# Optimization experiments

Measured on AMD Instinct MI355X. Metric: run time of the kernel, lower is better.

Reference implementation:

```python
import jax, jax.numpy as jnp
import numpy as np
import math

D = 2048
NH = 16
HD = D // NH
MULT = 4
EPS = 1e-6


def rmsnorm(x, g):
    norm = jax.lax.rsqrt(jnp.mean(x * x, axis=-1, keepdims=True) + EPS)
    return g * x * norm


def setup_inputs() -> dict:
    key = jax.random.key(0)
    ks = jax.random.split(key, 8)
    s = 0.02  # keep activations in a sane range
    return {
        "x": jax.random.normal(ks[0], (2, 2048, D), dtype=jnp.float32),
        "g1": jnp.ones((D,), dtype=jnp.float32),
        "wq": jax.random.normal(ks[1], (D, D), dtype=jnp.float32) * s,
        "wk": jax.random.normal(ks[2], (D, D), dtype=jnp.float32) * s,
        "wv": jax.random.normal(ks[3], (D, D), dtype=jnp.float32) * s,
        "wo": jax.random.normal(ks[4], (D, D), dtype=jnp.float32) * s,
        "g2": jnp.ones((D,), dtype=jnp.float32),
        "w_up": jax.random.normal(ks[5], (2 * D * MULT, D), dtype=jnp.float32) * s,
        "w_down": jax.random.normal(ks[6], (D, D * MULT), dtype=jnp.float32) * s,
    }


def reference(x, g1, wq, wk, wv, wo, g2, w_up, w_down):
    B, T, _ = x.shape
    # --- causal self-attention with pre-RMSNorm ---
    h = rmsnorm(x, g1)
    q = (h @ wq.T).reshape(B, T, NH, HD).transpose(0, 2, 1, 3)  # [B,H,T,hd]
    k = (h @ wk.T).reshape(B, T, NH, HD).transpose(0, 2, 1, 3)
    v = (h @ wv.T).reshape(B, T, NH, HD).transpose(0, 2, 1, 3)
    att = jnp.einsum("bhtd,bhsd->bhts", q, k) / math.sqrt(HD)  # [B,H,T,T]
    neg = jnp.finfo(att.dtype).min
    causal = jnp.triu(jnp.full((T, T), neg, dtype=att.dtype), k=1)
    att = att + causal
    w = jax.nn.softmax(att, axis=-1)
    z = jnp.einsum("bhts,bhsd->bhtd", w, v)  # [B,H,T,hd]
    z = z.transpose(0, 2, 1, 3).reshape(B, T, D)
    x = x + z @ wo.T
    # --- SwiGLU-style FFN (GELU gate) with pre-RMSNorm ---
    h2 = rmsnorm(x, g2)
    uv = h2 @ w_up.T  # [B,T,2*D*MULT]
    u, vgate = jnp.split(uv, 2, axis=-1)
    ff = (jax.nn.gelu(u, approximate=False) * vgate) @ w_down.T
    return x + ff
```

## Files before the change

kernel.cpp:

```cpp
#include <hip/hip_runtime.h>
#include <math.h>

typedef __bf16 bf16_t;
typedef __bf16 bf16x8 __attribute__((ext_vector_type(8)));
typedef __bf16 bf16x4 __attribute__((ext_vector_type(4)));
typedef float f32x4 __attribute__((ext_vector_type(4)));

#define D_MODEL 2048
#define N_HEADS 16
#define HEAD_D 128
#define SEQ 2048
#define NTOK 4096
#define DFF 8192
#define UPN 16384

#define GLDS16(g, l) __builtin_amdgcn_global_load_lds( \
    (const __attribute__((address_space(1))) void*)(g), \
    (__attribute__((address_space(3))) void*)(l), 16, 0, 0)

#define MFMA16(a, b, c) __builtin_amdgcn_mfma_f32_16x16x32_bf16((a), (b), (c), 0, 0, 0)

__global__ __launch_bounds__(256) void cvt_bf16_kernel(const float* __restrict__ in,
                                                       bf16_t* __restrict__ out, long n4) {
    long i = (long)blockIdx.x * 256 + threadIdx.x;
    long stride = (long)gridDim.x * 256;
    for (; i < n4; i += stride) {
        float4 f = ((const float4*)in)[i];
        bf16x4 v;
        v[0] = (bf16_t)f.x; v[1] = (bf16_t)f.y; v[2] = (bf16_t)f.z; v[3] = (bf16_t)f.w;
        ((bf16x4*)out)[i] = v;
    }
}

__global__ __launch_bounds__(256) void rmsnorm_kernel(const float* __restrict__ x,
                                                      const float* __restrict__ g,
                                                      bf16_t* __restrict__ out) {
    int row = blockIdx.x;
    const float* xr = x + (size_t)row * D_MODEL;
    int c0 = threadIdx.x * 8;
    float4 a = *(const float4*)&xr[c0];
    float4 b = *(const float4*)&xr[c0 + 4];
    float ss = a.x*a.x + a.y*a.y + a.z*a.z + a.w*a.w
             + b.x*b.x + b.y*b.y + b.z*b.z + b.w*b.w;
    #pragma unroll
    for (int off = 1; off < 64; off <<= 1) ss += __shfl_xor(ss, off);
    __shared__ float red[4];
    if ((threadIdx.x & 63) == 0) red[threadIdx.x >> 6] = ss;
    __syncthreads();
    float norm = rsqrtf((red[0] + red[1] + red[2] + red[3]) * (1.f / D_MODEL) + 1e-6f);
    float4 ga = *(const float4*)&g[c0];
    float4 gb = *(const float4*)&g[c0 + 4];
    bf16x8 o;
    o[0] = (bf16_t)(a.x * ga.x * norm); o[1] = (bf16_t)(a.y * ga.y * norm);
    o[2] = (bf16_t)(a.z * ga.z * norm); o[3] = (bf16_t)(a.w * ga.w * norm);
    o[4] = (bf16_t)(b.x * gb.x * norm); o[5] = (bf16_t)(b.y * gb.y * norm);
    o[6] = (bf16_t)(b.z * gb.z * norm); o[7] = (bf16_t)(b.w * gb.w * norm);
    *(bf16x8*)&out[(size_t)row * D_MODEL + c0] = o;
}

__global__ __launch_bounds__(256) void combine3_kernel(const float* __restrict__ r,
        const float* __restrict__ p0, const float* __restrict__ p1,
        float* __restrict__ out, long n4) {
    long i = (long)blockIdx.x * 256 + threadIdx.x;
    long stride = (long)gridDim.x * 256;
    for (; i < n4; i += stride) {
        float4 a = ((const float4*)r)[i];
        float4 b = ((const float4*)p0)[i];
        float4 c = ((const float4*)p1)[i];
        float4 o; o.x = a.x+b.x+c.x; o.y = a.y+b.y+c.y; o.z = a.z+b.z+c.z; o.w = a.w+b.w+c.w;
        ((float4*)out)[i] = o;
    }
}

template<int MODE, int KSPLIT>
__global__ __launch_bounds__(512, 2)
void gemm256(const bf16_t* __restrict__ A, const bf16_t* __restrict__ W,
             void* __restrict__ o0, void* __restrict__ o1, void* __restrict__ o2,
             const float* __restrict__ res, int nbx, int K)
{
    __shared__ __align__(16) bf16_t ldsA[4 * 8192];
    __shared__ __align__(16) bf16_t ldsB[4 * 8192];
    const int tid = threadIdx.x;
    const int wave = tid >> 6, lane = tid & 63;
    const int lr = lane & 15, lg = lane >> 4;
    const int wm = wave >> 2, wn = wave & 3;

    const int nwg = gridDim.x, bid = blockIdx.x;
    const int cpx = nwg >> 3;
    const int s = (bid & 7) * cpx + (bid >> 3);
    const int by = s & 15, bx = s >> 4;
    const int bm0 = by * 256;
    const int bn0 = (MODE == 2) ? bx * 128 : bx * 256;
    const int z = (KSPLIT == 2) ? blockIdx.z : 0;
    const int Keff = K / KSPLIT;
    const int koff = z * Keff;

    const int rl0 = wave * 16 + (lane >> 2);
    const int Lof = ((lane & 3) ^ ((rl0 >> 1) & 3)) * 8;
    const bf16_t* asrc0 = A + (size_t)(bm0 + rl0) * K + koff + Lof;
    const bf16_t* asrc1 = asrc0 + (size_t)128 * K;
    const bf16_t* bsrc0;
    const bf16_t* bsrc1;
    if constexpr (MODE == 2) {
        int grp = rl0 >> 6, wi = rl0 & 63;
        int brow = (wi < 32) ? (bn0 + grp * 32 + wi) : (DFF + bn0 + grp * 32 + (wi - 32));
        bsrc0 = W + (size_t)brow * K + koff + Lof;
        bsrc1 = bsrc0 + (size_t)64 * K;
    } else {
        bsrc0 = W + (size_t)(bn0 + rl0) * K + koff + Lof;
        bsrc1 = bsrc0 + (size_t)128 * K;
    }

    auto issueA = [&](int t, int kh) {
        char* dst = (char*)ldsA + (((t & 1) * 2 + kh) * 16384) + wave * 1024;
        const bf16_t* sp = asrc0 + (size_t)t * 64 + kh * 32;
        GLDS16(sp, dst);
        GLDS16(asrc1 + (size_t)t * 64 + kh * 32, dst + 8192);
    };
    auto issueB = [&](int t, int kh) {
        char* dst = (char*)ldsB + (((t & 1) * 2 + kh) * 16384) + wave * 1024;
        GLDS16(bsrc0 + (size_t)t * 64 + kh * 32, dst);
        GLDS16(bsrc1 + (size_t)t * 64 + kh * 32, dst + 8192);
    };

    f32x4 acc[8][4] = {};
    const int xg = (lg ^ ((lr >> 1) & 3)) * 8;
    const int arow = wm * 128 + lr;
    const int brow = wn * 64 + lr;
    const int NKT = Keff >> 6;

    issueA(0, 0); issueB(0, 0); issueA(0, 1); issueB(0, 1);

#define HALF_BODY(J, ISSUE, KH, WC)                                                     \
    {                                                                                   \
        bf16x8 af[8], bfr[2];                                                           \
        const bf16_t* Ar = ldsA + (((J) & 1) * 2 + (KH)) * 8192;                        \
        const bf16_t* Br = ldsB + (((J) & 1) * 2 + (KH)) * 8192;                        \
        if (ISSUE) issueA((J) + 1, (KH));                                               \
        asm volatile("s_waitcnt vmcnt(" WC ")" ::: "memory");                           \
        __builtin_amdgcn_s_barrier();                                                   \
        _Pragma("unroll")                                                               \
        for (int m = 0; m < 8; ++m) af[m] = *(const bf16x8*)&Ar[(arow + m * 16) * 32 + xg]; \
        _Pragma("unroll")                                                               \
        for (int n = 0; n < 2; ++n) bfr[n] = *(const bf16x8*)&Br[(brow + n * 16) * 32 + xg]; \
        __builtin_amdgcn_s_setprio(1);                                                  \
        _Pragma("unroll")                                                               \
        for (int m = 0; m < 8; ++m) {                                                   \
            acc[m][0] = MFMA16(af[m], bfr[0], acc[m][0]);                               \
            acc[m][1] = MFMA16(af[m], bfr[1], acc[m][1]);                               \
        }                                                                               \
        __builtin_amdgcn_s_setprio(0);                                                  \
        if (ISSUE) issueB((J) + 1, (KH));                                               \
        _Pragma("unroll")                                                               \
        for (int n = 0; n < 2; ++n) bfr[n] = *(const bf16x8*)&Br[(brow + (n + 2) * 16) * 32 + xg]; \
        __builtin_amdgcn_s_setprio(1);                                                  \
        _Pragma("unroll")                                                               \
        for (int m = 0; m < 8; ++m) {                                                   \
            acc[m][2] = MFMA16(af[m], bfr[0], acc[m][2]);                               \
            acc[m][3] = MFMA16(af[m], bfr[1], acc[m][3]);                               \
        }                                                                               \
        __builtin_amdgcn_s_setprio(0);                                                  \
        __builtin_amdgcn_s_barrier();                                                   \
    }

    for (int j = 0; j < NKT - 1; ++j) {
        HALF_BODY(j, true, 0, "6");
        HALF_BODY(j, true, 1, "6");
    }
    HALF_BODY(NKT - 1, false, 0, "4");
    HALF_BODY(NKT - 1, false, 1, "0");
#undef HALF_BODY

    if constexpr (MODE == 0) {
        const float qs = 0.08838834764831845f;
        const int th = bn0 >> 11;
        #pragma unroll
        for (int m = 0; m < 8; ++m) {
            int grow = bm0 + wm * 128 + m * 16 + lg * 4;
            #pragma unroll
            for (int n = 0; n < 4; ++n) {
                int gcol = bn0 + wn * 64 + n * 16 + lr;
                int c = gcol & 2047;
                if (th == 0) {
                    #pragma unroll
                    for (int r = 0; r < 4; ++r)
                        ((bf16_t*)o0)[(size_t)(grow + r) * D_MODEL + c] = (bf16_t)(acc[m][n][r] * qs);
                } else if (th == 1) {
                    #pragma unroll
                    for (int r = 0; r < 4; ++r)
                        ((bf16_t*)o1)[(size_t)(grow + r) * D_MODEL + c] = (bf16_t)acc[m][n][r];
                } else {
                    int hh = c >> 7, d = c & 127;
                    int bb = grow >> 11, t0 = grow & 2047;
                    bf16x4 st;
                    #pragma unroll
                    for (int r = 0; r < 4; ++r) st[r] = (bf16_t)acc[m][n][r];
                    *(bf16x4*)&((bf16_t*)o2)[((size_t)(bb * N_HEADS + hh) * HEAD_D + d) * SEQ + t0] = st;
                }
            }
        }
    } else if constexpr (MODE == 1) {
        float* po = (KSPLIT == 2) ? ((float*)o0 + (size_t)z * NTOK * D_MODEL) : (float*)o0;
        #pragma unroll
        for (int m = 0; m < 8; ++m) {
            int grow = bm0 + wm * 128 + m * 16 + lg * 4;
            #pragma unroll
            for (int n = 0; n < 4; ++n) {
                int gcol = bn0 + wn * 64 + n * 16 + lr;
                #pragma unroll
                for (int r = 0; r < 4; ++r) {
                    size_t idx = (size_t)(grow + r) * D_MODEL + gcol;
                    if (KSPLIT == 2) po[idx] = acc[m][n][r];
                    else             po[idx] = res[idx] + acc[m][n][r];
                }
            }
        }
    } else {
        #pragma unroll
        for (int m = 0; m < 8; ++m) {
            int grow = bm0 + wm * 128 + m * 16 + lg * 4;
            #pragma unroll
            for (int n = 0; n < 2; ++n) {
                int gcol = bn0 + wn * 32 + n * 16 + lr;
                #pragma unroll
                for (int r = 0; r < 4; ++r) {
                    float u = acc[m][n][r], vg = acc[m][n + 2][r];
                    float ge = 0.5f * u * (1.f + erff(u * 0.70710678118654752f));
                    ((bf16_t*)o0)[(size_t)(grow + r) * DFF + gcol] = (bf16_t)(ge * vg);
                }
            }
        }
    }
}

__global__ __launch_bounds__(256)
void attn_kernel(const bf16_t* __restrict__ Q, const bf16_t* __restrict__ K,
                 const bf16_t* __restrict__ Vt, bf16_t* __restrict__ Z)
{
    const int qt = gridDim.x - 1 - blockIdx.x;
    const int h = blockIdx.y, b = blockIdx.z;
    const int q0 = qt * 64;
    const int tid = threadIdx.x, wave = tid >> 6, lane = tid & 63;
    const int lr = lane & 15, lg = lane >> 4;

    __shared__ __align__(16) bf16_t Qs[64 * 136];
    __shared__ __align__(16) bf16_t Ks[64 * 136];
    __shared__ __align__(16) bf16_t Vts[128 * 72];
    __shared__ __align__(16) bf16_t Ps[4][16 * 72];

    const size_t base = ((size_t)b * SEQ) * D_MODEL + (size_t)h * HEAD_D;
    const size_t vbase = (size_t)(b * N_HEADS + h) * HEAD_D * SEQ;

    #pragma unroll
    for (int i = 0; i < 4; ++i) {
        int v = tid + 256 * i;
        int row = v >> 4, cv = (v & 15) * 8;
        *(uint4*)&Qs[row * 136 + cv] = *(const uint4*)&Q[base + (size_t)(q0 + row) * D_MODEL + cv];
    }

    f32x4 o[8] = {};
    float mrun[4], lrun[4];
    #pragma unroll
    for (int r = 0; r < 4; ++r) { mrun[r] = -1e30f; lrun[r] = 0.f; }

    for (int kt = 0; kt <= qt; ++kt) {
        const int k0 = kt * 64;
        __syncthreads();
        #pragma unroll
        for (int i = 0; i < 4; ++i) {
            int v = tid + 256 * i;
            int row = v >> 4, cv = (v & 15) * 8;
            *(uint4*)&Ks[row * 136 + cv] = *(const uint4*)&K[base + (size_t)(k0 + row) * D_MODEL + cv];
            int d = v >> 3, c8 = (v & 7) * 8;
            *(uint4*)&Vts[d * 72 + c8] = *(const uint4*)&Vt[vbase + (size_t)d * SEQ + k0 + c8];
        }
        __syncthreads();

        f32x4 sv[4] = {};
        #pragma unroll
        for (int kk = 0; kk < 4; ++kk) {
            bf16x8 aq = *(const bf16x8*)&Qs[(wave * 16 + lr) * 136 + kk * 32 + lg * 8];
            #pragma unroll
            for (int nb = 0; nb < 4; ++nb) {
                bf16x8 bk = *(const bf16x8*)&Ks[(nb * 16 + lr) * 136 + kk * 32 + lg * 8];
                sv[nb] = MFMA16(aq, bk, sv[nb]);
            }
        }
        if (kt == qt) {
            #pragma unroll
            for (int nb = 0; nb < 4; ++nb)
                #pragma unroll
                for (int r = 0; r < 4; ++r) {
                    int qrel = 16 * wave + lg * 4 + r;
                    int krel = nb * 16 + lr;
                    if (krel > qrel) sv[nb][r] = -1e30f;
                }
        }
        float resc[4];
        #pragma unroll
        for (int r = 0; r < 4; ++r) {
            float mx = fmaxf(fmaxf(sv[0][r], sv[1][r]), fmaxf(sv[2][r], sv[3][r]));
            #pragma unroll
            for (int off = 1; off < 16; off <<= 1) mx = fmaxf(mx, __shfl_xor(mx, off));
            float mnew = fmaxf(mrun[r], mx);
            resc[r] = __expf(mrun[r] - mnew);
            float sum = 0.f;
            #pragma unroll
            for (int nb = 0; nb < 4; ++nb) {
                float p = __expf(sv[nb][r] - mnew);
                sv[nb][r] = p;
                sum += p;
            }
            #pragma unroll
            for (int off = 1; off < 16; off <<= 1) sum += __shfl_xor(sum, off);
            lrun[r] = lrun[r] * resc[r] + sum;
            mrun[r] = mnew;
        }
        #pragma unroll
        for (int ob = 0; ob < 8; ++ob)
            #pragma unroll
            for (int r = 0; r < 4; ++r) o[ob][r] *= resc[r];
        #pragma unroll
        for (int nb = 0; nb < 4; ++nb)
            #pragma unroll
            for (int r = 0; r < 4; ++r)
                Ps[wave][(lg * 4 + r) * 72 + nb * 16 + lr] = (bf16_t)sv[nb][r];
        #pragma unroll
        for (int kk = 0; kk < 2; ++kk) {
            bf16x8 ap = *(const bf16x8*)&Ps[wave][lr * 72 + kk * 32 + lg * 8];
            #pragma unroll
            for (int ob = 0; ob < 8; ++ob) {
                bf16x8 bv = *(const bf16x8*)&Vts[(ob * 16 + lr) * 72 + kk * 32 + lg * 8];
                o[ob] = MFMA16(ap, bv, o[ob]);
            }
        }
    }
    #pragma unroll
    for (int ob = 0; ob < 8; ++ob)
        #pragma unroll
        for (int r = 0; r < 4; ++r) {
            int t = q0 + 16 * wave + lg * 4 + r;
            Z[base + (size_t)t * D_MODEL + ob * 16 + lr] = (bf16_t)(o[ob][r] / lrun[r]);
        }
}

extern "C" void kernel_launch(void* const* d_in, const int* in_sizes, int n_in,
                              void* d_out, int out_size, void* d_ws, size_t ws_size,
                              hipStream_t stream)
{
    const float* x   = (const float*)d_in[0];
    const float* g1  = (const float*)d_in[1];
    const float* wq  = (const float*)d_in[2];
    const float* wk  = (const float*)d_in[3];
    const float* wv  = (const float*)d_in[4];
    const float* wo  = (const float*)d_in[5];
    const float* g2  = (const float*)d_in[6];
    const float* wup = (const float*)d_in[7];
    const float* wdn = (const float*)d_in[8];
    float* out = (float*)d_out;

    char* wsp = (char*)d_ws;
    size_t off = 0;
    auto alloc = [&](size_t bytes) { void* p = wsp + off; off += (bytes + 255) & ~255ull; return p; };
    bf16_t* wq_b  = (bf16_t*)alloc((size_t)D_MODEL * D_MODEL * 2);
    bf16_t* wk_b  = (bf16_t*)alloc((size_t)D_MODEL * D_MODEL * 2);
    bf16_t* wv_b  = (bf16_t*)alloc((size_t)D_MODEL * D_MODEL * 2);
    bf16_t* wo_b  = (bf16_t*)alloc((size_t)D_MODEL * D_MODEL * 2);
    bf16_t* wup_b = (bf16_t*)alloc((size_t)UPN * D_MODEL * 2);
    bf16_t* wdn_b = (bf16_t*)alloc((size_t)D_MODEL * DFF * 2);
    bf16_t* h_b   = (bf16_t*)alloc((size_t)NTOK * D_MODEL * 2);
    bf16_t* q_b   = (bf16_t*)alloc((size_t)NTOK * D_MODEL * 2);
    bf16_t* k_b   = (bf16_t*)alloc((size_t)NTOK * D_MODEL * 2);
    bf16_t* vt_b  = (bf16_t*)alloc((size_t)NTOK * D_MODEL * 2);
    bf16_t* z_b   = (bf16_t*)alloc((size_t)NTOK * D_MODEL * 2);
    float*  x1    = (float*) alloc((size_t)NTOK * D_MODEL * 4);
    bf16_t* h2_b  = (bf16_t*)alloc((size_t)NTOK * D_MODEL * 2);
    bf16_t* act_b = (bf16_t*)alloc((size_t)NTOK * DFF * 2);
    float* pbuf = (float*)h_b;

    auto cvt = [&](const float* in, bf16_t* outb, long n) {
        long n4 = n / 4;
        long nb = (n4 + 255) / 256;
        int blocks = nb > 2048 ? 2048 : (int)nb;
        cvt_bf16_kernel<<<blocks, 256, 0, stream>>>(in, outb, n4);
    };
    cvt(wq,  wq_b,  (long)D_MODEL * D_MODEL);
    cvt(wk,  wk_b,  (long)D_MODEL * D_MODEL);
    cvt(wv,  wv_b,  (long)D_MODEL * D_MODEL);
    cvt(wo,  wo_b,  (long)D_MODEL * D_MODEL);
    cvt(wup, wup_b, (long)UPN * D_MODEL);
    cvt(wdn, wdn_b, (long)D_MODEL * DFF);

    rmsnorm_kernel<<<NTOK, 256, 0, stream>>>(x, g1, h_b);

    gemm256<0, 1><<<24 * 16, 512, 0, stream>>>(h_b, wq_b, q_b, k_b, vt_b, nullptr, 24, D_MODEL);

    attn_kernel<<<dim3(SEQ / 64, N_HEADS, 2), 256, 0, stream>>>(q_b, k_b, vt_b, z_b);

    gemm256<1, 1><<<8 * 16, 512, 0, stream>>>(z_b, wo_b, x1, nullptr, nullptr, x, 8, D_MODEL);

    rmsnorm_kernel<<<NTOK, 256, 0, stream>>>(x1, g2, h2_b);

    gemm256<2, 1><<<64 * 16, 512, 0, stream>>>(h2_b, wup_b, act_b, nullptr, nullptr, nullptr, 64, D_MODEL);

    gemm256<1, 2><<<dim3(8 * 16, 1, 2), 512, 0, stream>>>(act_b, wdn_b, pbuf, nullptr, nullptr, nullptr, 8, DFF);
    combine3_kernel<<<2048, 256, 0, stream>>>(x1, pbuf, pbuf + (size_t)NTOK * D_MODEL, out,
                                              (long)NTOK * D_MODEL / 4);
}
```

Baseline: 1.076 ms.

## Restructure GEMM mainloop into quarter-phase pipeline and split-K the Wo projection

```diff
diff --git a/kernel.cpp b/kernel.cpp
--- a/kernel.cpp
+++ b/kernel.cpp
@@ -78,8 +78,8 @@
              void* __restrict__ o0, void* __restrict__ o1, void* __restrict__ o2,
              const float* __restrict__ res, int nbx, int K)
 {
-    __shared__ __align__(16) bf16_t ldsA[4 * 8192];
-    __shared__ __align__(16) bf16_t ldsB[4 * 8192];
+    __shared__ __align__(16) bf16_t ldsA[2 * 2 * 8192];
+    __shared__ __align__(16) bf16_t ldsB[2 * 2 * 8192];
     const int tid = threadIdx.x;
     const int wave = tid >> 6, lane = tid & 63;
     const int lr = lane & 15, lg = lane >> 4;
@@ -92,84 +92,125 @@
     const int bm0 = by * 256;
     const int bn0 = (MODE == 2) ? bx * 128 : bx * 256;
     const int z = (KSPLIT == 2) ? blockIdx.z : 0;
-    const int Keff = K / KSPLIT;
-    const int koff = z * Keff;
-
-    const int rl0 = wave * 16 + (lane >> 2);
-    const int Lof = ((lane & 3) ^ ((rl0 >> 1) & 3)) * 8;
-    const bf16_t* asrc0 = A + (size_t)(bm0 + rl0) * K + koff + Lof;
-    const bf16_t* asrc1 = asrc0 + (size_t)128 * K;
-    const bf16_t* bsrc0;
-    const bf16_t* bsrc1;
+    const int Keff = K / KSPLIT, koff = z * Keff;
+
+    const int rl = wave * 16 + (lane >> 2);
+    const int gsw = ((lane & 3) ^ ((rl >> 1) & 3)) * 8;
+    const bf16_t* asrc = A + (size_t)(bm0 + rl) * K + koff + gsw;
+    const bf16_t* bsrc;
+    size_t bstep2;
     if constexpr (MODE == 2) {
-        int grp = rl0 >> 6, wi = rl0 & 63;
+        int grp = rl >> 6, wi = rl & 63;
         int brow = (wi < 32) ? (bn0 + grp * 32 + wi) : (DFF + bn0 + grp * 32 + (wi - 32));
-        bsrc0 = W + (size_t)brow * K + koff + Lof;
-        bsrc1 = bsrc0 + (size_t)64 * K;
+        bsrc = W + (size_t)brow * K + koff + gsw;
+        bstep2 = (size_t)64 * K;
     } else {
-        bsrc0 = W + (size_t)(bn0 + rl0) * K + koff + Lof;
-        bsrc1 = bsrc0 + (size_t)128 * K;
-    }
-
-    auto issueA = [&](int t, int kh) {
-        char* dst = (char*)ldsA + (((t & 1) * 2 + kh) * 16384) + wave * 1024;
-        const bf16_t* sp = asrc0 + (size_t)t * 64 + kh * 32;
-        GLDS16(sp, dst);
-        GLDS16(asrc1 + (size_t)t * 64 + kh * 32, dst + 8192);
+        bsrc = W + (size_t)(bn0 + rl) * K + koff + gsw;
+        bstep2 = (size_t)128 * K;
+    }
+
+    auto stA = [&](int t, int kh) {
+        char* d = (char*)ldsA + (((t & 1) * 2 + kh) * 16384) + wave * 1024 + lane * 16;
+        const bf16_t* sp = asrc + (size_t)t * 64 + kh * 32;
+        GLDS16(sp, d);
+        GLDS16(sp + (size_t)128 * K, d + 8192);
     };
-    auto issueB = [&](int t, int kh) {
-        char* dst = (char*)ldsB + (((t & 1) * 2 + kh) * 16384) + wave * 1024;
-        GLDS16(bsrc0 + (size_t)t * 64 + kh * 32, dst);
-        GLDS16(bsrc1 + (size_t)t * 64 + kh * 32, dst + 8192);
+    auto stB = [&](int t, int kh) {
+        char* d = (char*)ldsB + (((t & 1) * 2 + kh) * 16384) + wave * 1024 + lane * 16;
+        const bf16_t* sp = bsrc + (size_t)t * 64 + kh * 32;
+        GLDS16(sp, d);
+        GLDS16(sp + bstep2, d + 8192);
     };
 
     f32x4 acc[8][4] = {};
     const int xg = (lg ^ ((lr >> 1) & 3)) * 8;
-    const int arow = wm * 128 + lr;
-    const int brow = wn * 64 + lr;
     const int NKT = Keff >> 6;
 
-    issueA(0, 0); issueB(0, 0); issueA(0, 1); issueB(0, 1);
-
-#define HALF_BODY(J, ISSUE, KH, WC)                                                     \
-    {                                                                                   \
-        bf16x8 af[8], bfr[2];                                                           \
-        const bf16_t* Ar = ldsA + (((J) & 1) * 2 + (KH)) * 8192;                        \
-        const bf16_t* Br = ldsB + (((J) & 1) * 2 + (KH)) * 8192;                        \
-        if (ISSUE) issueA((J) + 1, (KH));                                               \
-        asm volatile("s_waitcnt vmcnt(" WC ")" ::: "memory");                           \
-        __builtin_amdgcn_s_barrier();                                                   \
-        _Pragma("unroll")                                                               \
-        for (int m = 0; m < 8; ++m) af[m] = *(const bf16x8*)&Ar[(arow + m * 16) * 32 + xg]; \
-        _Pragma("unroll")                                                               \
-        for (int n = 0; n < 2; ++n) bfr[n] = *(const bf16x8*)&Br[(brow + n * 16) * 32 + xg]; \
-        __builtin_amdgcn_s_setprio(1);                                                  \
-        _Pragma("unroll")                                                               \
-        for (int m = 0; m < 8; ++m) {                                                   \
-            acc[m][0] = MFMA16(af[m], bfr[0], acc[m][0]);                               \
-            acc[m][1] = MFMA16(af[m], bfr[1], acc[m][1]);                               \
-        }                                                                               \
-        __builtin_amdgcn_s_setprio(0);                                                  \
-        if (ISSUE) issueB((J) + 1, (KH));                                               \
-        _Pragma("unroll")                                                               \
-        for (int n = 0; n < 2; ++n) bfr[n] = *(const bf16x8*)&Br[(brow + (n + 2) * 16) * 32 + xg]; \
-        __builtin_amdgcn_s_setprio(1);                                                  \
-        _Pragma("unroll")                                                               \
-        for (int m = 0; m < 8; ++m) {                                                   \
-            acc[m][2] = MFMA16(af[m], bfr[0], acc[m][2]);                               \
-            acc[m][3] = MFMA16(af[m], bfr[1], acc[m][3]);                               \
-        }                                                                               \
-        __builtin_amdgcn_s_setprio(0);                                                  \
-        __builtin_amdgcn_s_barrier();                                                   \
-    }
-
-    for (int j = 0; j < NKT - 1; ++j) {
-        HALF_BODY(j, true, 0, "6");
-        HALF_BODY(j, true, 1, "6");
-    }
-    HALF_BODY(NKT - 1, false, 0, "4");
-    HALF_BODY(NKT - 1, false, 1, "0");
-#undef HALF_BODY
+    stA(0, 0); stA(0, 1); stB(0, 0); stB(0, 1); stA(1, 0);
+    asm volatile("s_waitcnt vmcnt(2)" ::: "memory");
+    __builtin_amdgcn_s_barrier();
+    __builtin_amdgcn_sched_barrier(0);
+
+    for (int t = 0; t < NKT; ++t) {
+        const bf16_t* Ab = ldsA + ((t & 1) * 2) * 8192;
+        const bf16_t* Bb = ldsB + ((t & 1) * 2) * 8192;
+        const bool s1 = (t + 1 < NKT), s2 = (t + 2 < NKT);
+        bf16x8 af[4], bfr[4];
+
+        #pragma unroll
+        for (int i = 0; i < 4; ++i)
+            af[i] = *(const bf16x8*)&Ab[(wm * 128 + i * 16 + lr) * 32 + xg];
+        #pragma unroll
+        for (int n = 0; n < 4; ++n)
+            bfr[n] = *(const bf16x8*)&Bb[(wn * 64 + n * 16 + lr) * 32 + xg];
+        if (s1) { stA(t + 1, 1); stB(t + 1, 0); }
+        __builtin_amdgcn_s_barrier();
+        __builtin_amdgcn_sched_barrier(0);
+        __builtin_amdgcn_s_setprio(1);
+        #pragma unroll
+        for (int i = 0; i < 4; ++i)
+            #pragma unroll
+            for (int n = 0; n < 4; ++n)
+                acc[i][n] = MFMA16(af[i], bfr[n], acc[i][n]);
+        __builtin_amdgcn_s_setprio(0);
+        __builtin_amdgcn_s_barrier();
+        __builtin_amdgcn_sched_barrier(0);
+
+        #pragma unroll
+        for (int i = 0; i < 4; ++i)
+            af[i] = *(const bf16x8*)&Ab[(wm * 128 + (i + 4) * 16 + lr) * 32 + xg];
+        if (s1) stB(t + 1, 1);
+        __builtin_amdgcn_s_barrier();
+        __builtin_amdgcn_sched_barrier(0);
+        __builtin_amdgcn_s_setprio(1);
+        #pragma unroll
+        for (int i = 0; i < 4; ++i)
+            #pragma unroll
+            for (int n = 0; n < 4; ++n)
+                acc[i + 4][n] = MFMA16(af[i], bfr[n], acc[i + 4][n]);
+        __builtin_amdgcn_s_setprio(0);
+        __builtin_amdgcn_s_barrier();
+        __builtin_amdgcn_sched_barrier(0);
+
+        #pragma unroll
+        for (int i = 0; i < 4; ++i)
+            af[i] = *(const bf16x8*)&Ab[8192 + (wm * 128 + i * 16 + lr) * 32 + xg];
+        #pragma unroll
+        for (int n = 0; n < 4; ++n)
+            bfr[n] = *(const bf16x8*)&Bb[8192 + (wn * 64 + n * 16 + lr) * 32 + xg];
+        __builtin_amdgcn_s_barrier();
+        __builtin_amdgcn_sched_barrier(0);
+        __builtin_amdgcn_s_setprio(1);
+        #pragma unroll
+        for (int i = 0; i < 4; ++i)
+            #pragma unroll
+            for (int n = 0; n < 4; ++n)
+                acc[i][n] = MFMA16(af[i], bfr[n], acc[i][n]);
+        __builtin_amdgcn_s_setprio(0);
+        __builtin_amdgcn_s_barrier();
+        __builtin_amdgcn_sched_barrier(0);
+
+        #pragma unroll
+        for (int i = 0; i < 4; ++i)
+            af[i] = *(const bf16x8*)&Ab[8192 + (wm * 128 + (i + 4) * 16 + lr) * 32 + xg];
+        if (s2) {
+            stA(t + 2, 0);
+            asm volatile("s_waitcnt vmcnt(2)" ::: "memory");
+        } else {
+            asm volatile("s_waitcnt vmcnt(0)" ::: "memory");
+        }
+        __builtin_amdgcn_s_barrier();
+        __builtin_amdgcn_sched_barrier(0);
+        __builtin_amdgcn_s_setprio(1);
+        #pragma unroll
+        for (int i = 0; i < 4; ++i)
+            #pragma unroll
+            for (int n = 0; n < 4; ++n)
+                acc[i + 4][n] = MFMA16(af[i], bfr[n], acc[i + 4][n]);
+        __builtin_amdgcn_s_setprio(0);
+        __builtin_amdgcn_s_barrier();
+        __builtin_amdgcn_sched_barrier(0);
+    }
 
     if constexpr (MODE == 0) {
         const float qs = 0.08838834764831845f;
@@ -397,7 +438,9 @@
 
     attn_kernel<<<dim3(SEQ / 64, N_HEADS, 2), 256, 0, stream>>>(q_b, k_b, vt_b, z_b);
 
-    gemm256<1, 1><<<8 * 16, 512, 0, stream>>>(z_b, wo_b, x1, nullptr, nullptr, x, 8, D_MODEL);
+    gemm256<1, 2><<<dim3(8 * 16, 1, 2), 512, 0, stream>>>(z_b, wo_b, pbuf, nullptr, nullptr, nullptr, 8, D_MODEL);
+    combine3_kernel<<<2048, 256, 0, stream>>>(x, pbuf, pbuf + (size_t)NTOK * D_MODEL, x1,
+                                              (long)NTOK * D_MODEL / 4);
 
     rmsnorm_kernel<<<NTOK, 256, 0, stream>>>(x1, g2, h2_b);
 
```

Result: faster. 1.054 ms (-2.0%).
